# Performance work log

Hardware: AMD Instinct MI355X
Metric: run time of the kernel (lower is better)

## Reference

```python
import jax, jax.numpy as jnp
import numpy as np
import math

B, L, HID = 2, 1024, 768
H, TOPK = 12, 32
D = HID // H


def setup_inputs() -> dict:
    key = jax.random.key(0)
    ks = jax.random.split(key, 8)
    return {
        "hidden_states": jax.random.normal(ks[0], (B, L, HID), jnp.float32),
        "rel_bbox_emb": jax.random.normal(ks[1], (B, L, TOPK, HID), jnp.float32),
        "rel_bbox_index": jax.random.randint(ks[2], (B, L, TOPK), 0, L),
        "attention_mask": jnp.zeros((B, 1, L, L), jnp.bool_),
        "rel_pos": jax.random.normal(ks[3], (B, H, L, L), jnp.float32),
        "rel_2d_pos": jax.random.normal(ks[4], (B, H, L, L), jnp.float32),
        "w_qkv": jax.random.normal(ks[5], (HID, 3 * HID), jnp.float32) * (HID ** -0.5),
        "q_bias": jnp.zeros((HID,), jnp.float32),
        "v_bias": jnp.zeros((HID,), jnp.float32),
        "w_rq": jax.random.normal(ks[6], (HID, HID), jnp.float32) * (HID ** -0.5),
        "b_rq": jnp.zeros((HID,), jnp.float32),
    }


def _heads(x):  # [B,L,HID] -> [B,H,L,D]
    b, l, _ = x.shape
    return x.reshape(b, l, H, D).transpose(0, 2, 1, 3)


def reference(hidden_states, rel_bbox_emb, rel_bbox_index, attention_mask,
              rel_pos, rel_2d_pos, w_qkv, q_bias, v_bias, w_rq, b_rq):
    b, l, hid = hidden_states.shape
    scale = 1.0 / math.sqrt(D)
    NEG = jnp.float32(-1e8)

    qkv = hidden_states @ w_qkv                     # [B,L,3*HID]
    q, k, v = jnp.split(qkv, 3, axis=-1)
    q = q + q_bias
    v = v + v_bias

    ql = _heads(q) * scale                          # [B,H,L,D]
    kl = _heads(k)
    vl = _heads(v)
    scores = jnp.einsum('bhid,bhjd->bhij', ql, kl)  # [B,H,L,L]

    # relative bbox bias: q_bbox . rel_bbox_emb over top-k neighbors, scatter-added
    qb = _heads(q @ w_rq + b_rq) * scale            # [B,H,L,D]
    rbe = rel_bbox_emb.reshape(b, l, TOPK, H, D).transpose(0, 3, 1, 2, 4)  # [B,H,L,T,D]
    bbox_scores = jnp.einsum('bhid,bhijd->bhij', qb, rbe)  # [B,H,L,T]

    bi = jnp.arange(b)[:, None, None, None]
    hi = jnp.arange(H)[None, :, None, None]
    li = jnp.arange(l)[None, None, :, None]
    ji = rel_bbox_index[:, None, :, :]              # [B,1,L,T] broadcast over heads
    scores = scores.at[bi, hi, li, ji].add(bbox_scores)

    # local attention: mask out all positions NOT in the top-k neighbor set
    local_mask = jnp.ones((b, H, l, l), jnp.bool_).at[bi, hi, li, ji].set(False)
    scores = jnp.where(local_mask, NEG, scores)

    scores = scores + rel_pos + rel_2d_pos
    scores = jnp.where(attention_mask, NEG, scores)

    probs = jax.nn.softmax(scores, axis=-1)
    ctx = jnp.einsum('bhij,bhjd->bhid', probs, vl)  # [B,H,L,D]
    ctx = ctx.transpose(0, 2, 1, 3).reshape(b, l, hid)
    return ctx
```

## Files before the change

kernel.cpp:

```cpp
#include <hip/hip_runtime.h>
#include <hip/hip_bf16.h>
#include <math.h>

#define B_    2
#define L_    1024
#define H_    12
#define D_    64
#define HID_  768
#define TOPK_ 32
#define NEG_  (-100000000.0f)

__global__ void prep_bias(const float* __restrict__ qb_,
                          const float* __restrict__ vb_,
                          float* __restrict__ biasq) {
    int n = blockIdx.x * 256 + threadIdx.x;
    if (n >= 3 * HID_) return;
    float v = 0.f;
    if (n < HID_) v = qb_[n];
    else if (n >= 2 * HID_) v = vb_[n - 2 * HID_];
    biasq[n] = v;
}

__global__ __launch_bounds__(256) void gemm_f32(
    const float* __restrict__ A, int lda,
    const float* __restrict__ Bm, int ldb,
    const float* __restrict__ bias,
    float* __restrict__ C, int ldc,
    int M, int N, int K)
{
    __shared__ __align__(16) float As[16][132];
    __shared__ __align__(16) float Bs[16][128];

    const int tid = threadIdx.x;
    const int tx = tid & 15, ty = tid >> 4;
    const int bn = blockIdx.x * 128;
    const int bm = blockIdx.y * 128;

    const int arow = tid >> 1;
    const int akq  = (tid & 1) * 8;
    const int bkr  = tid >> 4;
    const int bnq  = (tid & 15) * 8;

    const float* Aptr = A + (size_t)(bm + arow) * lda + akq;
    const float* Bptr = Bm + (size_t)bkr * ldb + bn + bnq;

    float acc[8][8];
#pragma unroll
    for (int r = 0; r < 8; ++r)
#pragma unroll
        for (int c = 0; c < 8; ++c) acc[r][c] = 0.f;

    float4 a0 = *(const float4*)(Aptr);
    float4 a1 = *(const float4*)(Aptr + 4);
    float4 b0 = *(const float4*)(Bptr);
    float4 b1 = *(const float4*)(Bptr + 4);

    for (int k0 = 0; k0 < K; k0 += 16) {
        __syncthreads();
        As[akq + 0][arow] = a0.x; As[akq + 1][arow] = a0.y;
        As[akq + 2][arow] = a0.z; As[akq + 3][arow] = a0.w;
        As[akq + 4][arow] = a1.x; As[akq + 5][arow] = a1.y;
        As[akq + 6][arow] = a1.z; As[akq + 7][arow] = a1.w;
        *(float4*)(&Bs[bkr][bnq])     = b0;
        *(float4*)(&Bs[bkr][bnq + 4]) = b1;
        __syncthreads();

        if (k0 + 16 < K) {
            a0 = *(const float4*)(Aptr + k0 + 16);
            a1 = *(const float4*)(Aptr + k0 + 20);
            b0 = *(const float4*)(Bptr + (size_t)(k0 + 16) * ldb);
            b1 = *(const float4*)(Bptr + (size_t)(k0 + 16) * ldb + 4);
        }

#pragma unroll
        for (int kk = 0; kk < 16; ++kk) {
            const float4 av0 = *(const float4*)(&As[kk][ty * 8]);
            const float4 av1 = *(const float4*)(&As[kk][ty * 8 + 4]);
            const float4 bv0 = *(const float4*)(&Bs[kk][tx * 8]);
            const float4 bv1 = *(const float4*)(&Bs[kk][tx * 8 + 4]);
            const float a_[8] = {av0.x, av0.y, av0.z, av0.w, av1.x, av1.y, av1.z, av1.w};
            const float b_[8] = {bv0.x, bv0.y, bv0.z, bv0.w, bv1.x, bv1.y, bv1.z, bv1.w};
#pragma unroll
            for (int r = 0; r < 8; ++r)
#pragma unroll
                for (int c = 0; c < 8; ++c)
                    acc[r][c] = fmaf(a_[r], b_[c], acc[r][c]);
        }
    }

    float bv[8];
#pragma unroll
    for (int c = 0; c < 8; ++c) bv[c] = bias ? bias[bn + tx * 8 + c] : 0.f;

#pragma unroll
    for (int r = 0; r < 8; ++r) {
        float* crow = C + (size_t)(bm + ty * 8 + r) * ldc + bn + tx * 8;
        float4 o0, o1;
        o0.x = acc[r][0] + bv[0]; o0.y = acc[r][1] + bv[1];
        o0.z = acc[r][2] + bv[2]; o0.w = acc[r][3] + bv[3];
        o1.x = acc[r][4] + bv[4]; o1.y = acc[r][5] + bv[5];
        o1.z = acc[r][6] + bv[6]; o1.w = acc[r][7] + bv[7];
        *(float4*)crow       = o0;
        *(float4*)(crow + 4) = o1;
    }
}

__global__ __launch_bounds__(384) void attn_kernel(
    const float* __restrict__ qkv,
    const float* __restrict__ qb,
    const float* __restrict__ rbe,
    const int*   __restrict__ ridx,
    const unsigned char* __restrict__ amask,
    const float* __restrict__ rel_pos,
    const float* __restrict__ rel2d,
    float* __restrict__ out)
{
    const int bi = blockIdx.x;
    const int b = bi >> 10, i = bi & (L_ - 1);
    const int tid = threadIdx.x;
    const float scale = 0.125f;

    __shared__ __align__(16) float sQ[HID_];
    __shared__ __align__(16) float sQb[HID_];
    __shared__ int   sIdx[TOPK_];
    __shared__ unsigned char sFirst[TOPK_];
    __shared__ float sBbox[H_][TOPK_ + 1];
    __shared__ float sScore[H_][TOPK_ + 1];
    __shared__ float sProb[H_][TOPK_ + 1];

    {
        const float* qrow  = qkv + (size_t)bi * (3 * HID_);
        const float* qbrow = qb + (size_t)bi * HID_;
        for (int d = tid; d < HID_; d += 384) {
            sQ[d]  = qrow[d]  * scale;
            sQb[d] = qbrow[d] * scale;
        }
        if (tid < TOPK_) sIdx[tid] = ridx[bi * TOPK_ + tid];
    }
    __syncthreads();

    if (tid < TOPK_) {
        int j = sIdx[tid];
        unsigned char f = 1;
        for (int t2 = 0; t2 < tid; ++t2)
            if (sIdx[t2] == j) { f = 0; break; }
        sFirst[tid] = f;
    }

    const int grp = tid >> 4;
    const int l16 = tid & 15;

#pragma unroll 4
    for (int it = 0; it < 16; ++it) {
        int p = it * 24 + grp;
        int t = p / 12, h = p - t * 12;
        const float4 r4 = *(const float4*)(rbe + (((size_t)bi * TOPK_ + t) * HID_) + h * D_ + l16 * 4);
        const float4 q4 = *(const float4*)(sQb + h * D_ + l16 * 4);
        float s = r4.x * q4.x + r4.y * q4.y + r4.z * q4.z + r4.w * q4.w;
        s += __shfl_xor(s, 1); s += __shfl_xor(s, 2);
        s += __shfl_xor(s, 4); s += __shfl_xor(s, 8);
        if (l16 == 0) sBbox[h][t] = s;
    }

#pragma unroll 4
    for (int it = 0; it < 16; ++it) {
        int p = it * 24 + grp;
        int t = p / 12, h = p - t * 12;
        int j = sIdx[t];
        const float4 k4 = *(const float4*)(qkv + (size_t)(b * L_ + j) * (3 * HID_) + HID_ + h * D_ + l16 * 4);
        const float4 q4 = *(const float4*)(sQ + h * D_ + l16 * 4);
        float s = k4.x * q4.x + k4.y * q4.y + k4.z * q4.z + k4.w * q4.w;
        s += __shfl_xor(s, 1); s += __shfl_xor(s, 2);
        s += __shfl_xor(s, 4); s += __shfl_xor(s, 8);
        if (l16 == 0) {
            size_t ro = (((size_t)(b * H_ + h)) * L_ + i) * L_ + j;
            s += rel_pos[ro] + rel2d[ro];
            sScore[h][t] = s;
        }
    }
    __syncthreads();

    {
        int h = tid >> 5;
        int t = tid & 31;
        int j = sIdx[t];
        float s = -INFINITY;
        if (sFirst[t]) {
            float bb = 0.f;
#pragma unroll
            for (int t2 = 0; t2 < TOPK_; ++t2)
                if (sIdx[t2] == j) bb += sBbox[h][t2];
            s = sScore[h][t] + bb;
            if (amask[((size_t)b * L_ + i) * L_ + j]) s = NEG_;
        }
        float m = s;
        m = fmaxf(m, __shfl_xor(m, 1));  m = fmaxf(m, __shfl_xor(m, 2));
        m = fmaxf(m, __shfl_xor(m, 4));  m = fmaxf(m, __shfl_xor(m, 8));
        m = fmaxf(m, __shfl_xor(m, 16));
        float e = expf(s - m);
        float sum = e;
        sum += __shfl_xor(sum, 1);  sum += __shfl_xor(sum, 2);
        sum += __shfl_xor(sum, 4);  sum += __shfl_xor(sum, 8);
        sum += __shfl_xor(sum, 16);
        sProb[h][t] = e / sum;
    }
    __syncthreads();

    {
        int h = tid >> 5;
        int dd = (tid & 31) * 2;
        float a0 = 0.f, a1 = 0.f;
#pragma unroll
        for (int t = 0; t < TOPK_; ++t) {
            float p = sProb[h][t];
            if (p != 0.f) {
                int j = sIdx[t];
                const float2 v2 = *(const float2*)(qkv + (size_t)(b * L_ + j) * (3 * HID_) + 2 * HID_ + h * D_ + dd);
                a0 = fmaf(p, v2.x, a0);
                a1 = fmaf(p, v2.y, a1);
            }
        }
        float2 o; o.x = a0; o.y = a1;
        *(float2*)(out + (size_t)bi * HID_ + h * D_ + dd) = o;
    }
}

extern "C" void kernel_launch(void* const* d_in, const int* in_sizes, int n_in,
                              void* d_out, int out_size, void* d_ws, size_t ws_size,
                              hipStream_t stream)
{
    const float* hidden  = (const float*)d_in[0];
    const float* rbe     = (const float*)d_in[1];
    const int*   ridx    = (const int*)d_in[2];
    const unsigned char* amask = (const unsigned char*)d_in[3];
    const float* rel_pos = (const float*)d_in[4];
    const float* rel2d   = (const float*)d_in[5];
    const float* w_qkv   = (const float*)d_in[6];
    const float* q_bias  = (const float*)d_in[7];
    const float* v_bias  = (const float*)d_in[8];
    const float* w_rq    = (const float*)d_in[9];
    const float* b_rq    = (const float*)d_in[10];
    float* out = (float*)d_out;

    const int M = B_ * L_;
    float* qkv   = (float*)d_ws;
    float* qb    = qkv + (size_t)M * (3 * HID_);
    float* biasq = qb + (size_t)M * HID_;

    prep_bias<<<9, 256, 0, stream>>>(q_bias, v_bias, biasq);

    dim3 g1((3 * HID_) / 128, M / 128);
    gemm_f32<<<g1, 256, 0, stream>>>(hidden, HID_, w_qkv, 3 * HID_, biasq,
                                     qkv, 3 * HID_, M, 3 * HID_, HID_);
    dim3 g2(HID_ / 128, M / 128);
    gemm_f32<<<g2, 256, 0, stream>>>(qkv, 3 * HID_, w_rq, HID_, b_rq,
                                     qb, HID_, M, HID_, HID_);

    attn_kernel<<<B_ * L_, 384, 0, stream>>>(qkv, qb, rbe, ridx, amask,
                                             rel_pos, rel2d, out);
}
```

Measured before the change: 672.4 us.

## Use split-bf16 MFMA GEMMs and restructure attention gather kernel

Replaces the FP32 SIMT GEMMs with bf16 MFMA GEMMs that recover near-FP32 accuracy by splitting each operand into high and low bf16 parts along a tripled K dimension (hi*hi + hi*lo + lo*hi). Extra kernels split and transpose activations and weights into swizzled bf16 buffers loaded directly into LDS. The attention kernel is also reworked so each thread computes a full per-(head, neighbor) dot product without shuffles, and the V rows are prefetched into registers before the softmax barrier. This trades extra conversion passes, a 3x larger K and higher register pressure for matrix-core throughput and better memory overlap.

```diff
diff --git a/kernel.cpp b/kernel.cpp
--- a/kernel.cpp
+++ b/kernel.cpp
@@ -9,6 +9,16 @@
 #define HID_  768
 #define TOPK_ 32
 #define NEG_  (-100000000.0f)
+#define KP_   2304
+
+typedef __attribute__((ext_vector_type(8))) short short8;
+typedef __attribute__((ext_vector_type(4))) short short4v;
+typedef __attribute__((ext_vector_type(4))) float f32x4;
+
+__device__ __forceinline__ void gload16(const void* g, void* l) {
+    __builtin_amdgcn_global_load_lds((const __attribute__((address_space(1))) void*)g,
+                                     (__attribute__((address_space(3))) void*)l, 16, 0, 0);
+}
 
 __global__ void prep_bias(const float* __restrict__ qb_,
                           const float* __restrict__ vb_,
@@ -21,87 +31,132 @@
     biasq[n] = v;
 }
 
-__global__ __launch_bounds__(256) void gemm_f32(
-    const float* __restrict__ A, int lda,
-    const float* __restrict__ Bm, int ldb,
+__global__ __launch_bounds__(256) void split_a(const float* __restrict__ src, int srcStride,
+                                               __hip_bfloat16* __restrict__ dst) {
+    int idx = blockIdx.x * 256 + threadIdx.x;
+    int r = idx / 192, c4 = (idx - r * 192) * 4;
+    const float4 x = *(const float4*)(src + (size_t)r * srcStride + c4);
+    float xs[4] = {x.x, x.y, x.z, x.w};
+    short4v h4, l4;
+#pragma unroll
+    for (int j = 0; j < 4; ++j) {
+        __hip_bfloat16 h = __float2bfloat16(xs[j]);
+        __hip_bfloat16 l = __float2bfloat16(xs[j] - __bfloat162float(h));
+        h4[j] = *(short*)&h;
+        l4[j] = *(short*)&l;
+    }
+    short* d = (short*)(dst + (size_t)r * KP_ + c4);
+    *(short4v*)(d)         = h4;
+    *(short4v*)(d + 768)   = h4;
+    *(short4v*)(d + 1536)  = l4;
+}
+
+__global__ __launch_bounds__(256) void split_w(const float* __restrict__ src, int N,
+                                               __hip_bfloat16* __restrict__ dst) {
+    __shared__ float tile[32][33];
+    const int n0 = blockIdx.x * 32, k0 = blockIdx.y * 32;
+    const int tx = threadIdx.x & 31, ty = threadIdx.x >> 5;
+#pragma unroll
+    for (int p = 0; p < 4; ++p) {
+        int r = p * 8 + ty;
+        tile[r][tx] = src[(size_t)(k0 + r) * N + n0 + tx];
+    }
+    __syncthreads();
+#pragma unroll
+    for (int p = 0; p < 4; ++p) {
+        int nl = p * 8 + ty;
+        float xv = tile[tx][nl];
+        __hip_bfloat16 h = __float2bfloat16(xv);
+        __hip_bfloat16 l = __float2bfloat16(xv - __bfloat162float(h));
+        size_t base = (size_t)(n0 + nl) * KP_ + k0 + tx;
+        dst[base]        = h;
+        dst[base + 768]  = l;
+        dst[base + 1536] = h;
+    }
+}
+
+template<int BM, int BN>
+__global__ __launch_bounds__(256) void gemm_split(
+    const __hip_bfloat16* __restrict__ A,
+    const __hip_bfloat16* __restrict__ Bt,
     const float* __restrict__ bias,
-    float* __restrict__ C, int ldc,
-    int M, int N, int K)
+    float* __restrict__ C, int ldc)
 {
-    __shared__ __align__(16) float As[16][132];
-    __shared__ __align__(16) float Bs[16][128];
-
-    const int tid = threadIdx.x;
-    const int tx = tid & 15, ty = tid >> 4;
-    const int bn = blockIdx.x * 128;
-    const int bm = blockIdx.y * 128;
-
-    const int arow = tid >> 1;
-    const int akq  = (tid & 1) * 8;
-    const int bkr  = tid >> 4;
-    const int bnq  = (tid & 15) * 8;
-
-    const float* Aptr = A + (size_t)(bm + arow) * lda + akq;
-    const float* Bptr = Bm + (size_t)bkr * ldb + bn + bnq;
-
-    float acc[8][8];
-#pragma unroll
-    for (int r = 0; r < 8; ++r)
-#pragma unroll
-        for (int c = 0; c < 8; ++c) acc[r][c] = 0.f;
-
-    float4 a0 = *(const float4*)(Aptr);
-    float4 a1 = *(const float4*)(Aptr + 4);
-    float4 b0 = *(const float4*)(Bptr);
-    float4 b1 = *(const float4*)(Bptr + 4);
-
-    for (int k0 = 0; k0 < K; k0 += 16) {
+    constexpr int NT  = KP_ / 64;
+    constexpr int ACH = BM / 32;
+    constexpr int BCH = BN / 32;
+    constexpr int MI  = BM / 32;
+    constexpr int NI  = BN / 32;
+    __shared__ __align__(16) char smem[(BM + BN) * 128];
+
+    const int tid  = threadIdx.x;
+    const int wid  = tid >> 6, lane = tid & 63;
+    const int wr   = wid >> 1, wc = wid & 1;
+    const int bm   = blockIdx.y * BM, bn = blockIdx.x * BN;
+    const int r4   = lane >> 4, l15 = lane & 15;
+
+    f32x4 acc[MI][NI];
+#pragma unroll
+    for (int mi = 0; mi < MI; ++mi)
+#pragma unroll
+        for (int ni = 0; ni < NI; ++ni) acc[mi][ni] = (f32x4){0.f, 0.f, 0.f, 0.f};
+
+    const char* Ab  = (const char*)A;
+    const char* Btb = (const char*)Bt;
+
+    for (int kt = 0; kt < NT; ++kt) {
         __syncthreads();
-        As[akq + 0][arow] = a0.x; As[akq + 1][arow] = a0.y;
-        As[akq + 2][arow] = a0.z; As[akq + 3][arow] = a0.w;
-        As[akq + 4][arow] = a1.x; As[akq + 5][arow] = a1.y;
-        As[akq + 6][arow] = a1.z; As[akq + 7][arow] = a1.w;
-        *(float4*)(&Bs[bkr][bnq])     = b0;
-        *(float4*)(&Bs[bkr][bnq + 4]) = b1;
+#pragma unroll
+        for (int c = 0; c < ACH; ++c) {
+            int slot = c * 4096 + tid * 16;
+            int R = slot >> 7, cb = (slot >> 4) & 7;
+            const char* g = Ab + (size_t)(bm + R) * (KP_ * 2) + kt * 128 + ((cb ^ (R & 7)) << 4);
+            gload16(g, smem + c * 4096 + wid * 1024);
+        }
+#pragma unroll
+        for (int c = 0; c < BCH; ++c) {
+            int slot = c * 4096 + tid * 16;
+            int R = slot >> 7, cb = (slot >> 4) & 7;
+            const char* g = Btb + (size_t)(bn + R) * (KP_ * 2) + kt * 128 + ((cb ^ (R & 7)) << 4);
+            gload16(g, smem + BM * 128 + c * 4096 + wid * 1024);
+        }
         __syncthreads();
 
-        if (k0 + 16 < K) {
-            a0 = *(const float4*)(Aptr + k0 + 16);
-            a1 = *(const float4*)(Aptr + k0 + 20);
-            b0 = *(const float4*)(Bptr + (size_t)(k0 + 16) * ldb);
-            b1 = *(const float4*)(Bptr + (size_t)(k0 + 16) * ldb + 4);
-        }
-
-#pragma unroll
-        for (int kk = 0; kk < 16; ++kk) {
-            const float4 av0 = *(const float4*)(&As[kk][ty * 8]);
-            const float4 av1 = *(const float4*)(&As[kk][ty * 8 + 4]);
-            const float4 bv0 = *(const float4*)(&Bs[kk][tx * 8]);
-            const float4 bv1 = *(const float4*)(&Bs[kk][tx * 8 + 4]);
-            const float a_[8] = {av0.x, av0.y, av0.z, av0.w, av1.x, av1.y, av1.z, av1.w};
-            const float b_[8] = {bv0.x, bv0.y, bv0.z, bv0.w, bv1.x, bv1.y, bv1.z, bv1.w};
-#pragma unroll
-            for (int r = 0; r < 8; ++r)
-#pragma unroll
-                for (int c = 0; c < 8; ++c)
-                    acc[r][c] = fmaf(a_[r], b_[c], acc[r][c]);
-        }
-    }
-
-    float bv[8];
-#pragma unroll
-    for (int c = 0; c < 8; ++c) bv[c] = bias ? bias[bn + tx * 8 + c] : 0.f;
-
-#pragma unroll
-    for (int r = 0; r < 8; ++r) {
-        float* crow = C + (size_t)(bm + ty * 8 + r) * ldc + bn + tx * 8;
-        float4 o0, o1;
-        o0.x = acc[r][0] + bv[0]; o0.y = acc[r][1] + bv[1];
-        o0.z = acc[r][2] + bv[2]; o0.w = acc[r][3] + bv[3];
-        o1.x = acc[r][4] + bv[4]; o1.y = acc[r][5] + bv[5];
-        o1.z = acc[r][6] + bv[6]; o1.w = acc[r][7] + bv[7];
-        *(float4*)crow       = o0;
-        *(float4*)(crow + 4) = o1;
+#pragma unroll
+        for (int kk = 0; kk < 2; ++kk) {
+            short8 af[MI], bfv[NI];
+#pragma unroll
+            for (int mi = 0; mi < MI; ++mi) {
+                int m_loc = wr * (BM / 2) + mi * 16 + l15;
+                int off = (m_loc * 128 + kk * 64 + r4 * 16) ^ ((m_loc & 7) << 4);
+                af[mi] = *(const short8*)(smem + off);
+            }
+#pragma unroll
+            for (int ni = 0; ni < NI; ++ni) {
+                int n_loc = wc * (BN / 2) + ni * 16 + l15;
+                int off = BM * 128 + ((n_loc * 128 + kk * 64 + r4 * 16) ^ ((n_loc & 7) << 4));
+                bfv[ni] = *(const short8*)(smem + off);
+            }
+#pragma unroll
+            for (int mi = 0; mi < MI; ++mi)
+#pragma unroll
+                for (int ni = 0; ni < NI; ++ni)
+                    acc[mi][ni] = __builtin_amdgcn_mfma_f32_16x16x32_bf16(
+                        af[mi], bfv[ni], acc[mi][ni], 0, 0, 0);
+        }
+    }
+
+#pragma unroll
+    for (int mi = 0; mi < MI; ++mi) {
+        int row = bm + wr * (BM / 2) + mi * 16 + r4 * 4;
+#pragma unroll
+        for (int ni = 0; ni < NI; ++ni) {
+            int col = bn + wc * (BN / 2) + ni * 16 + l15;
+            float bv = bias[col];
+#pragma unroll
+            for (int reg = 0; reg < 4; ++reg)
+                C[(size_t)(row + reg) * ldc + col] = acc[mi][ni][reg] + bv;
+        }
     }
 }
 
@@ -118,15 +173,18 @@
     const int bi = blockIdx.x;
     const int b = bi >> 10, i = bi & (L_ - 1);
     const int tid = threadIdx.x;
+    const int h = tid >> 5, t = tid & 31;
     const float scale = 0.125f;
 
     __shared__ __align__(16) float sQ[HID_];
     __shared__ __align__(16) float sQb[HID_];
     __shared__ int   sIdx[TOPK_];
     __shared__ unsigned char sFirst[TOPK_];
-    __shared__ float sBbox[H_][TOPK_ + 1];
-    __shared__ float sScore[H_][TOPK_ + 1];
-    __shared__ float sProb[H_][TOPK_ + 1];
+    __shared__ unsigned char sMask[TOPK_];
+    __shared__ float sRel[H_][TOPK_];
+    __shared__ float sBbox[H_][TOPK_];
+    __shared__ float sScore[H_][TOPK_];
+    __shared__ float sProb[H_][TOPK_];
 
     {
         const float* qrow  = qkv + (size_t)bi * (3 * HID_);
@@ -139,51 +197,70 @@
     }
     __syncthreads();
 
-    if (tid < TOPK_) {
-        int j = sIdx[tid];
-        unsigned char f = 1;
-        for (int t2 = 0; t2 < tid; ++t2)
-            if (sIdx[t2] == j) { f = 0; break; }
-        sFirst[tid] = f;
-    }
-
-    const int grp = tid >> 4;
-    const int l16 = tid & 15;
-
-#pragma unroll 4
-    for (int it = 0; it < 16; ++it) {
-        int p = it * 24 + grp;
-        int t = p / 12, h = p - t * 12;
-        const float4 r4 = *(const float4*)(rbe + (((size_t)bi * TOPK_ + t) * HID_) + h * D_ + l16 * 4);
-        const float4 q4 = *(const float4*)(sQb + h * D_ + l16 * 4);
-        float s = r4.x * q4.x + r4.y * q4.y + r4.z * q4.z + r4.w * q4.w;
-        s += __shfl_xor(s, 1); s += __shfl_xor(s, 2);
-        s += __shfl_xor(s, 4); s += __shfl_xor(s, 8);
-        if (l16 == 0) sBbox[h][t] = s;
-    }
-
-#pragma unroll 4
-    for (int it = 0; it < 16; ++it) {
-        int p = it * 24 + grp;
-        int t = p / 12, h = p - t * 12;
-        int j = sIdx[t];
-        const float4 k4 = *(const float4*)(qkv + (size_t)(b * L_ + j) * (3 * HID_) + HID_ + h * D_ + l16 * 4);
-        const float4 q4 = *(const float4*)(sQ + h * D_ + l16 * 4);
-        float s = k4.x * q4.x + k4.y * q4.y + k4.z * q4.z + k4.w * q4.w;
-        s += __shfl_xor(s, 1); s += __shfl_xor(s, 2);
-        s += __shfl_xor(s, 4); s += __shfl_xor(s, 8);
-        if (l16 == 0) {
-            size_t ro = (((size_t)(b * H_ + h)) * L_ + i) * L_ + j;
-            s += rel_pos[ro] + rel2d[ro];
-            sScore[h][t] = s;
-        }
+    const int j = sIdx[t];
+
+    {
+        size_t ro = (((size_t)(b * H_ + h)) * L_ + i) * L_ + j;
+        sRel[h][t] = rel_pos[ro] + rel2d[ro];
+        if (tid < TOPK_) {
+            int jj = sIdx[tid];
+            sMask[tid] = amask[((size_t)b * L_ + i) * L_ + jj];
+            unsigned char f = 1;
+            for (int t2 = 0; t2 < tid; ++t2)
+                if (sIdx[t2] == jj) { f = 0; break; }
+            sFirst[tid] = f;
+        }
+    }
+
+    {
+        const float* rrow = rbe + ((size_t)bi * TOPK_ + t) * HID_ + h * D_;
+        const float* krow = qkv + (size_t)(b * L_ + j) * (3 * HID_) + HID_ + h * D_;
+        const float* qbh  = sQb + h * D_;
+        const float* qh   = sQ + h * D_;
+        float accB0 = 0.f, accB1 = 0.f, accB2 = 0.f, accB3 = 0.f;
+        float accK0 = 0.f, accK1 = 0.f, accK2 = 0.f, accK3 = 0.f;
+#pragma unroll
+        for (int it = 0; it < 16; it += 4) {
+            const float4 r0 = *(const float4*)(rrow + (it + 0) * 4);
+            const float4 r1 = *(const float4*)(rrow + (it + 1) * 4);
+            const float4 r2 = *(const float4*)(rrow + (it + 2) * 4);
+            const float4 r3 = *(const float4*)(rrow + (it + 3) * 4);
+            const float4 k0 = *(const float4*)(krow + (it + 0) * 4);
+            const float4 k1 = *(const float4*)(krow + (it + 1) * 4);
+            const float4 k2 = *(const float4*)(krow + (it + 2) * 4);
+            const float4 k3 = *(const float4*)(krow + (it + 3) * 4);
+            const float4 qb0 = *(const float4*)(qbh + (it + 0) * 4);
+            const float4 qb1 = *(const float4*)(qbh + (it + 1) * 4);
+            const float4 qb2 = *(const float4*)(qbh + (it + 2) * 4);
+            const float4 qb3 = *(const float4*)(qbh + (it + 3) * 4);
+            const float4 q0 = *(const float4*)(qh + (it + 0) * 4);
+            const float4 q1 = *(const float4*)(qh + (it + 1) * 4);
+            const float4 q2 = *(const float4*)(qh + (it + 2) * 4);
+            const float4 q3 = *(const float4*)(qh + (it + 3) * 4);
+            accB0 = fmaf(r0.x, qb0.x, fmaf(r0.y, qb0.y, fmaf(r0.z, qb0.z, fmaf(r0.w, qb0.w, accB0))));
+            accB1 = fmaf(r1.x, qb1.x, fmaf(r1.y, qb1.y, fmaf(r1.z, qb1.z, fmaf(r1.w, qb1.w, accB1))));
+            accB2 = fmaf(r2.x, qb2.x, fmaf(r2.y, qb2.y, fmaf(r2.z, qb2.z, fmaf(r2.w, qb2.w, accB2))));
+            accB3 = fmaf(r3.x, qb3.x, fmaf(r3.y, qb3.y, fmaf(r3.z, qb3.z, fmaf(r3.w, qb3.w, accB3))));
+            accK0 = fmaf(k0.x, q0.x, fmaf(k0.y, q0.y, fmaf(k0.z, q0.z, fmaf(k0.w, q0.w, accK0))));
+            accK1 = fmaf(k1.x, q1.x, fmaf(k1.y, q1.y, fmaf(k1.z, q1.z, fmaf(k1.w, q1.w, accK1))));
+            accK2 = fmaf(k2.x, q2.x, fmaf(k2.y, q2.y, fmaf(k2.z, q2.z, fmaf(k2.w, q2.w, accK2))));
+            accK3 = fmaf(k3.x, q3.x, fmaf(k3.y, q3.y, fmaf(k3.z, q3.z, fmaf(k3.w, q3.w, accK3))));
+        }
+        sBbox[h][t]  = (accB0 + accB1) + (accB2 + accB3);
+        sScore[h][t] = (accK0 + accK1) + (accK2 + accK3) + sRel[h][t];
+    }
+
+    const int dd = (t) * 2;
+    float2 vpre[TOPK_];
+    {
+        const float* vbase = qkv + (size_t)b * L_ * (3 * HID_) + 2 * HID_ + h * D_ + dd;
+#pragma unroll
+        for (int tt = 0; tt < TOPK_; ++tt)
+            vpre[tt] = *(const float2*)(vbase + (size_t)sIdx[tt] * (3 * HID_));
     }
     __syncthreads();
 
     {
-        int h = tid >> 5;
-        int t = tid & 31;
-        int j = sIdx[t];
         float s = -INFINITY;
         if (sFirst[t]) {
             float bb = 0.f;
@@ -191,7 +268,7 @@
             for (int t2 = 0; t2 < TOPK_; ++t2)
                 if (sIdx[t2] == j) bb += sBbox[h][t2];
             s = sScore[h][t] + bb;
-            if (amask[((size_t)b * L_ + i) * L_ + j]) s = NEG_;
+            if (sMask[t]) s = NEG_;
         }
         float m = s;
         m = fmaxf(m, __shfl_xor(m, 1));  m = fmaxf(m, __shfl_xor(m, 2));
@@ -207,18 +284,12 @@
     __syncthreads();
 
     {
-        int h = tid >> 5;
-        int dd = (tid & 31) * 2;
         float a0 = 0.f, a1 = 0.f;
 #pragma unroll
-        for (int t = 0; t < TOPK_; ++t) {
-            float p = sProb[h][t];
-            if (p != 0.f) {
-                int j = sIdx[t];
-                const float2 v2 = *(const float2*)(qkv + (size_t)(b * L_ + j) * (3 * HID_) + 2 * HID_ + h * D_ + dd);
-                a0 = fmaf(p, v2.x, a0);
-                a1 = fmaf(p, v2.y, a1);
-            }
+        for (int tt = 0; tt < TOPK_; ++tt) {
+            float p = sProb[h][tt];
+            a0 = fmaf(p, vpre[tt].x, a0);
+            a1 = fmaf(p, vpre[tt].y, a1);
         }
         float2 o; o.x = a0; o.y = a1;
         *(float2*)(out + (size_t)bi * HID_ + h * D_ + dd) = o;
@@ -243,18 +314,27 @@
     float* out = (float*)d_out;
 
     const int M = B_ * L_;
-    float* qkv   = (float*)d_ws;
-    float* qb    = qkv + (size_t)M * (3 * HID_);
-    float* biasq = qb + (size_t)M * HID_;
+    char* ws = (char*)d_ws;
+    float* qkv   = (float*)(ws);
+    float* qb    = (float*)(ws + 18874368);
+    float* biasq = (float*)(ws + 25165824);
+    __hip_bfloat16* A1  = (__hip_bfloat16*)(ws + 25175040);
+    __hip_bfloat16* A2  = (__hip_bfloat16*)(ws + 34612224);
+    __hip_bfloat16* Bt1 = (__hip_bfloat16*)(ws + 44049408);
+    __hip_bfloat16* Bt2 = (__hip_bfloat16*)(ws + 54666240);
 
     prep_bias<<<9, 256, 0, stream>>>(q_bias, v_bias, biasq);
-
-    dim3 g1((3 * HID_) / 128, M / 128);
-    gemm_f32<<<g1, 256, 0, stream>>>(hidden, HID_, w_qkv, 3 * HID_, biasq,
-                                     qkv, 3 * HID_, M, 3 * HID_, HID_);
-    dim3 g2(HID_ / 128, M / 128);
-    gemm_f32<<<g2, 256, 0, stream>>>(qkv, 3 * HID_, w_rq, HID_, b_rq,
-                                     qb, HID_, M, HID_, HID_);
+    split_a<<<1536, 256, 0, stream>>>(hidden, HID_, A1);
+    split_w<<<dim3(2304 / 32, 768 / 32), 256, 0, stream>>>(w_qkv, 3 * HID_, Bt1);
+    split_w<<<dim3(768 / 32, 768 / 32), 256, 0, stream>>>(w_rq, HID_, Bt2);
+
+    gemm_split<128, 64><<<dim3((3 * HID_) / 64, M / 128), 256, 0, stream>>>(
+        A1, Bt1, biasq, qkv, 3 * HID_);
+
+    split_a<<<1536, 256, 0, stream>>>(qkv, 3 * HID_, A2);
+
+    gemm_split<64, 64><<<dim3(HID_ / 64, M / 64), 256, 0, stream>>>(
+        A2, Bt2, b_rq, qb, HID_);
 
     attn_kernel<<<B_ * L_, 384, 0, stream>>>(qkv, qb, rbe, ridx, amask,
                                              rel_pos, rel2d, out);
```

Measured after the change: 542.2 us. -19.4%, faster.
